# Kernel tuning notes

Measured on AMD Instinct MI355X. Metric: run time of the kernel, lower is better.

## Reference

```python
import jax, jax.numpy as jnp
import numpy as np

B, T_FRAMES, N, D, H, HT = 2, 16, 256, 768, 12, 12
INNER = 2 * D  # ConditionedTransitionBlock expansion_factor=2

def _ln(x, eps=1e-5):
    m = jnp.mean(x, axis=-1, keepdims=True)
    v = jnp.var(x, axis=-1, keepdims=True)
    return (x - m) * jax.lax.rsqrt(v + eps)

def _adaln(a, s, snorm_w, scale_w, scale_b, shift_w):
    an = _ln(a)            # LayerNorm(dim), no affine
    sn = _ln(s) * snorm_w  # LayerNorm(dim_cond), weight only
    return jax.nn.sigmoid(sn @ scale_w + scale_b) * an + sn @ shift_w

def _forward(a, s, bias, timestamps,
             ada_snorm_w, ada_scale_w, ada_scale_b, ada_shift_w,
             pb_q_w, pb_q_b, pb_k_w, pb_v_w, pb_g_w, pb_o_w,
             op_w, op_b,
             tr_snorm_w, tr_scale_w, tr_scale_b, tr_shift_w,
             tr_gate_w, tr_ab_w, tr_ba_w, tr_out_w, tr_out_b,
             tmp_ln_w, tmp_ln_b, tmp_q_w, tmp_q_b, tmp_k_w, tmp_v_w,
             tmp_decay, tmp_o_w,
             mask, multiplicity, T):
    BT, Nn, Dd = a.shape
    Bb = BT // T
    dh = Dd // H
    # --- AdaLN ---
    b = _adaln(a, s, ada_snorm_w, ada_scale_w, ada_scale_b, ada_shift_w)
    # --- pair-bias spatial attention (compute_pair_bias=False: z already (B,N,N,H)) ---
    q = (b @ pb_q_w + pb_q_b).reshape(BT, Nn, H, dh)
    k = (b @ pb_k_w).reshape(BT, Nn, H, dh)
    v = (b @ pb_v_w).reshape(BT, Nn, H, dh)
    z = jnp.transpose(bias, (0, 3, 1, 2))     # (B, H, N, N)
    z = jnp.repeat(z, multiplicity, axis=0)   # expand over T -> (B*T, H, N, N)
    scores = jnp.einsum('bqhd,bkhd->bhqk', q, k) * (dh ** -0.5) + z
    scores = jnp.where(mask[:, None, None, :], scores, -1e6)
    attn = jax.nn.softmax(scores, axis=-1)
    o = jnp.einsum('bhqk,bkhd->bqhd', attn, v).reshape(BT, Nn, Dd)
    g = jax.nn.sigmoid(b @ pb_g_w)
    attn_out = (g * o) @ pb_o_w
    # gated output projection (sigmoid, weights init 0 / bias -2) multiplied into residual
    a = a + jax.nn.sigmoid(s @ op_w + op_b) * attn_out
    # --- temporal attention with decay over T frames ---
    x = a.reshape(Bb, T, Nn, Dd).transpose(0, 2, 1, 3)   # (B, N, T, D)
    h = _ln(x) * tmp_ln_w + tmp_ln_b
    dht = Dd // HT
    qt = (h @ tmp_q_w + tmp_q_b).reshape(Bb, Nn, T, HT, dht)
    kt = (h @ tmp_k_w).reshape(Bb, Nn, T, HT, dht)
    vt = (h @ tmp_v_w).reshape(Bb, Nn, T, HT, dht)
    dt = jnp.abs(timestamps[:, :, None] - timestamps[:, None, :])           # (B, T, T)
    tb = -jax.nn.softplus(tmp_decay)[None, :, None, None] * dt[:, None]     # (B, HT, T, T)
    sct = jnp.einsum('bnqhd,bnkhd->bnhqk', qt, kt) * (dht ** -0.5) + tb[:, None]
    att = jax.nn.softmax(sct, axis=-1)
    ot = jnp.einsum('bnhqk,bnkhd->bnqhd', att, vt).reshape(Bb, Nn, T, Dd) @ tmp_o_w
    x = x + ot  # residual inside temporal attention
    a = x.transpose(0, 2, 1, 3).reshape(BT, Nn, Dd)
    # --- conditioned transition (SwiGLU gated by sigmoid(Linear(s))) ---
    b2 = _adaln(a, s, tr_snorm_w, tr_scale_w, tr_scale_b, tr_shift_w)
    hid = jax.nn.silu(b2 @ tr_gate_w) * (b2 @ tr_ab_w)
    a = a + jax.nn.sigmoid(s @ tr_out_w + tr_out_b) * (hid @ tr_ba_w)
    return a  # post_layer_norm=False -> Identity

def setup_inputs():
    key = jax.random.key(0)
    ks = iter(jax.random.split(key, 48))
    f = lambda shape, sc=1.0: jax.random.normal(next(ks), shape, jnp.float32) * sc
    return {
        'a': f((B * T_FRAMES, N, D)),
        's': f((B * T_FRAMES, N, D)),
        'bias': f((B, N, N, H)),
        'mask': jnp.ones((B * T_FRAMES, N), dtype=bool),
        'timestamps': jnp.sort(jax.random.uniform(next(ks), (B, T_FRAMES)) * 10.0, axis=-1),
        'multiplicity': T_FRAMES,
        'T': T_FRAMES,
        'ada_snorm_w': jnp.ones((D,)), 'ada_scale_w': f((D, D), 0.02),
        'ada_scale_b': jnp.zeros((D,)), 'ada_shift_w': f((D, D), 0.02),
        'pb_q_w': f((D, D), 0.02), 'pb_q_b': jnp.zeros((D,)),
        'pb_k_w': f((D, D), 0.02), 'pb_v_w': f((D, D), 0.02),
        'pb_g_w': f((D, D), 0.02), 'pb_o_w': f((D, D), 0.02),
        'op_w': f((D, D), 0.02), 'op_b': jnp.full((D,), -2.0),
        'tr_snorm_w': jnp.ones((D,)), 'tr_scale_w': f((D, D), 0.02),
        'tr_scale_b': jnp.zeros((D,)), 'tr_shift_w': f((D, D), 0.02),
        'tr_gate_w': f((D, INNER), 0.02), 'tr_ab_w': f((D, INNER), 0.02),
        'tr_ba_w': f((INNER, D), 0.02),
        'tr_out_w': f((D, D), 0.02), 'tr_out_b': jnp.full((D,), -2.0),
        'tmp_ln_w': jnp.ones((D,)), 'tmp_ln_b': jnp.zeros((D,)),
        'tmp_q_w': f((D, D), 0.02), 'tmp_q_b': jnp.zeros((D,)),
        'tmp_k_w': f((D, D), 0.02), 'tmp_v_w': f((D, D), 0.02),
        'tmp_decay': jnp.full((HT,), 0.5), 'tmp_o_w': f((D, D), 0.02),
    }

def reference(a, s, bias, mask, timestamps, multiplicity, T,
              ada_snorm_w, ada_scale_w, ada_scale_b, ada_shift_w,
              pb_q_w, pb_q_b, pb_k_w, pb_v_w, pb_g_w, pb_o_w,
              op_w, op_b,
              tr_snorm_w, tr_scale_w, tr_scale_b, tr_shift_w,
              tr_gate_w, tr_ab_w, tr_ba_w, tr_out_w, tr_out_b,
              tmp_ln_w, tmp_ln_b, tmp_q_w, tmp_q_b, tmp_k_w, tmp_v_w,
              tmp_decay, tmp_o_w):
    return _forward(a, s, bias, timestamps,
                    ada_snorm_w, ada_scale_w, ada_scale_b, ada_shift_w,
                    pb_q_w, pb_q_b, pb_k_w, pb_v_w, pb_g_w, pb_o_w,
                    op_w, op_b,
                    tr_snorm_w, tr_scale_w, tr_scale_b, tr_shift_w,
                    tr_gate_w, tr_ab_w, tr_ba_w, tr_out_w, tr_out_b,
                    tmp_ln_w, tmp_ln_b, tmp_q_w, tmp_q_b, tmp_k_w, tmp_v_w,
                    tmp_decay, tmp_o_w,
                    mask, multiplicity, T)
```

## Files before the change

### kernel.cpp

```cpp
#include <hip/hip_runtime.h>

typedef short s16x8 __attribute__((ext_vector_type(8)));
typedef short s16x4 __attribute__((ext_vector_type(4)));
typedef float f32x4 __attribute__((ext_vector_type(4)));
typedef __bf16 bf16x8 __attribute__((ext_vector_type(8)));

__device__ __forceinline__ float bf2f(short u) {
  union { unsigned int i; float f; } c;
  c.i = ((unsigned int)(unsigned short)u) << 16;
  return c.f;
}
__device__ __forceinline__ short f2bf(float f) {
  union { float f; unsigned int i; } c; c.f = f;
  unsigned int r = c.i + 0x7FFFu + ((c.i >> 16) & 1u);
  return (short)(r >> 16);
}
__device__ __forceinline__ float sigmoidf_(float x) { return 1.f / (1.f + __expf(-x)); }

template <typename T>
__device__ __forceinline__ auto mfma_sel(T a, T b, f32x4 c, int)
    -> decltype(__builtin_amdgcn_mfma_f32_16x16x32_bf16(a, b, c, 0, 0, 0)) {
  return __builtin_amdgcn_mfma_f32_16x16x32_bf16(a, b, c, 0, 0, 0);
}
template <typename T>
__device__ __forceinline__ f32x4 mfma_sel(T a, T b, f32x4 c, long) {
  return __builtin_amdgcn_mfma_f32_16x16x32_bf16(
      __builtin_bit_cast(bf16x8, a), __builtin_bit_cast(bf16x8, b), c, 0, 0, 0);
}
__device__ __forceinline__ f32x4 MFMA16(s16x8 a, s16x8 b, f32x4 c) {
  return mfma_sel(a, b, c, 0);
}

__device__ __forceinline__ void gl2lds16(const void* g, void* l) {
  __builtin_amdgcn_global_load_lds(
      (const __attribute__((address_space(1))) unsigned int*)g,
      (__attribute__((address_space(3))) unsigned int*)l, 16, 0, 0);
}

__device__ __forceinline__ int xcd_swz(int id, int nwg) {
  int q = nwg >> 3, r = nwg & 7;
  int xcd = id & 7, idx = id >> 3;
  return (xcd < r ? xcd * (q + 1) : r * (q + 1) + (xcd - r) * q) + idx;
}

__device__ __forceinline__ void tile_mn(int nid, int gx, int* mt, int* nt) {
  int sb = nid / (gx << 3);
  int rem = nid - sb * (gx << 3);
  *mt = (sb << 3) + (rem & 7);
  *nt = rem >> 3;
}

#define OFF_WADA1    0u
#define OFF_WQKVG    2359296u
#define OFF_WO       7077888u
#define OFF_WGATES   8257536u
#define OFF_WTMPQKV  10616832u
#define OFF_WTMPO    14155776u
#define OFF_WADA2    15335424u
#define OFF_WTRANS   17694720u
#define OFF_WBA      22413312u
#define OFF_BIAS     24772608u
#define OFF_ZT       24812544u
#define OFF_AN1      31104000u
#define OFF_SN1      43686912u
#define OFF_SN2      56269824u
#define OFF_SBF      68852736u
#define OFF_CADA     81435648u
#define OFF_QKVG     106601472u
#define OFF_GATES    156933120u
#define OFF_OGO      182098944u
#define OFF_A1       194681856u

__global__ __launch_bounds__(256) void prep_all(
    const float* p0, const float* p1, const float* p2, const float* p3,
    const float* p4, const float* p5, const float* p6, const float* p7,
    const float* p8, const float* p9, const float* p10, const float* p11,
    const float* p12, const float* p13, const float* p14, const float* p15,
    const float* p16, const float* p17, short* wsb,
    const float* __restrict__ zsrc, const float* __restrict__ ada_scale_b,
    const float* __restrict__ pb_q_b, const float* __restrict__ op_b,
    const float* __restrict__ tr_out_b, const float* __restrict__ tmp_q_b,
    const float* __restrict__ tr_scale_b,
    float* __restrict__ biasbuf, short* __restrict__ zt,
    const float* __restrict__ a_in, const float* __restrict__ s_in,
    const float* __restrict__ lnw1, const float* __restrict__ lnw2,
    short* __restrict__ an1, short* __restrict__ sn1, short* __restrict__ sn2,
    short* __restrict__ sbf) {
  const int z = blockIdx.z;
  const int tid = threadIdx.y * 32 + threadIdx.x;
  if (z < 18) {
    struct E { int K, N, dst; };
    const E tab[18] = {
        {768, 768, 0},        {768, 768, 589824},
        {768, 768, 1179648},  {768, 768, 1769472},
        {768, 768, 2359296},  {768, 768, 2949120},
        {768, 768, 3538944},
        {768, 768, 4128768},  {768, 768, 4718592},
        {768, 768, 7667712},  {768, 768, 8257536},
        {768, 1536, 8847360}, {768, 1536, 10027008},
        {1536, 768, 11206656},
        {768, 768, 5308416},  {768, 768, 5898240}, {768, 768, 6488064},
        {768, 768, 7077888}};
    int K = tab[z].K, N = tab[z].N;
    int n0 = blockIdx.x << 5, k0 = blockIdx.y << 5;
    if (n0 >= N || k0 >= K) return;
    const float* src;
    switch (z) {
      case 0: src = p0; break;  case 1: src = p1; break;
      case 2: src = p2; break;  case 3: src = p3; break;
      case 4: src = p4; break;  case 5: src = p5; break;
      case 6: src = p6; break;  case 7: src = p7; break;
      case 8: src = p8; break;  case 9: src = p9; break;
      case 10: src = p10; break; case 11: src = p11; break;
      case 12: src = p12; break; case 13: src = p13; break;
      case 14: src = p14; break; case 15: src = p15; break;
      case 16: src = p16; break; default: src = p17; break;
    }
    short* dst = wsb + tab[z].dst;
    __shared__ float tile[32][33];
    int tx = threadIdx.x, ty = threadIdx.y;
#pragma unroll
    for (int j = 0; j < 4; j++)
      tile[ty + j * 8][tx] = src[(long)(k0 + ty + j * 8) * N + n0 + tx];
    __syncthreads();
#pragma unroll
    for (int j = 0; j < 4; j++)
      dst[(long)(n0 + ty + j * 8) * K + k0 + tx] = f2bf(tile[tx][ty + j * 8]);
  } else if (z == 18) {
    const int bid = blockIdx.y * 48 + blockIdx.x;
    if (bid < 512) {
      const int b = bid >> 8, qq = bid & 255;
      const float* src = zsrc + (long)bid * 3072 + tid * 12;
      f32x4 v0 = *(const f32x4*)(src);
      f32x4 v1 = *(const f32x4*)(src + 4);
      f32x4 v2 = *(const f32x4*)(src + 8);
      float vals[12] = {v0[0], v0[1], v0[2], v0[3], v1[0], v1[1],
                        v1[2], v1[3], v2[0], v2[1], v2[2], v2[3]};
#pragma unroll
      for (int h = 0; h < 12; h++)
        zt[(((long)(b * 12 + h) * 256 + qq) << 8) + tid] = f2bf(vals[h]);
    } else if (bid < 551) {
      int j = (bid - 512) * 256 + tid;
      if (j < 9984) {
        float v;
        if (j < 1536) v = (j < 768) ? ada_scale_b[j] : 0.f;
        else if (j < 4608) { int jj = j - 1536; v = (jj < 768) ? pb_q_b[jj] : 0.f; }
        else if (j < 6144) { int jj = j - 4608; v = (jj < 768) ? op_b[jj] : tr_out_b[jj - 768]; }
        else if (j < 8448) { int jj = j - 6144; v = (jj < 768) ? tmp_q_b[jj] : 0.f; }
        else { int jj = j - 8448; v = (jj < 768) ? tr_scale_b[jj] : 0.f; }
        biasbuf[j] = v;
      }
    }
  } else {
    const int bid = blockIdx.y * 48 + blockIdx.x;
    if (bid >= 2048) return;
    const int wave = tid >> 6, lane = tid & 63;
    const int row = (bid << 2) + wave;
    const float* ar = a_in + (long)row * 768;
    const float* sr = s_in + (long)row * 768;
    f32x4 av[3], sv[3];
    float s0 = 0, s1 = 0, s2 = 0, s3 = 0;
#pragma unroll
    for (int k = 0; k < 3; k++) {
      int col = (lane << 2) + (k << 8);
      av[k] = *(const f32x4*)(ar + col);
      sv[k] = *(const f32x4*)(sr + col);
#pragma unroll
      for (int e = 0; e < 4; e++) {
        s0 += av[k][e]; s1 += av[k][e] * av[k][e];
        s2 += sv[k][e]; s3 += sv[k][e] * sv[k][e];
      }
    }
#pragma unroll
    for (int o = 32; o; o >>= 1) {
      s0 += __shfl_xor(s0, o, 64); s1 += __shfl_xor(s1, o, 64);
      s2 += __shfl_xor(s2, o, 64); s3 += __shfl_xor(s3, o, 64);
    }
    const float inv768 = 1.f / 768.f;
    float ma = s0 * inv768, va = s1 * inv768 - ma * ma;
    float ia = rsqrtf(va + 1e-5f);
    float ms = s2 * inv768, vs = s3 * inv768 - ms * ms;
    float is_ = rsqrtf(vs + 1e-5f);
#pragma unroll
    for (int k = 0; k < 3; k++) {
      int col = (lane << 2) + (k << 8);
      long o = (long)row * 768 + col;
      s16x4 o1, o2, o3, o4;
#pragma unroll
      for (int e = 0; e < 4; e++) {
        o1[e] = f2bf((av[k][e] - ma) * ia);
        float sn = (sv[k][e] - ms) * is_;
        o2[e] = f2bf(sn * lnw1[col + e]);
        o3[e] = f2bf(sn * lnw2[col + e]);
        o4[e] = f2bf(sv[k][e]);
      }
      *(s16x4*)(an1 + o) = o1;
      *(s16x4*)(sn1 + o) = o2;
      *(s16x4*)(sn2 + o) = o3;
      *(s16x4*)(sbf + o) = o4;
    }
  }
}

__global__ __launch_bounds__(256) void ln_affine(
    const float* __restrict__ in, const float* __restrict__ w,
    const float* __restrict__ b, short* __restrict__ out) {
  const int wave = threadIdx.x >> 6, lane = threadIdx.x & 63;
  const int row = (blockIdx.x << 2) + wave;
  const float* xr = in + (long)row * 768;
  f32x4 xv[3];
  float s0 = 0, s1 = 0;
#pragma unroll
  for (int k = 0; k < 3; k++) {
    int col = (lane << 2) + (k << 8);
    xv[k] = *(const f32x4*)(xr + col);
#pragma unroll
    for (int e = 0; e < 4; e++) { s0 += xv[k][e]; s1 += xv[k][e] * xv[k][e]; }
  }
#pragma unroll
  for (int o = 32; o; o >>= 1) { s0 += __shfl_xor(s0, o, 64); s1 += __shfl_xor(s1, o, 64); }
  const float inv768 = 1.f / 768.f;
  float m = s0 * inv768, v = s1 * inv768 - m * m;
  float inv = rsqrtf(v + 1e-5f);
#pragma unroll
  for (int k = 0; k < 3; k++) {
    int col = (lane << 2) + (k << 8);
    s16x4 p;
#pragma unroll
    for (int e = 0; e < 4; e++) {
      float y = (xv[k][e] - m) * inv;
      if (w) y = y * w[col + e] + b[col + e];
      p[e] = f2bf(y);
    }
    *(s16x4*)(out + (long)row * 768 + col) = p;
  }
}

template <int EP>
__device__ __forceinline__ void dev_gemm_bt(
    short* lds,
    const short* __restrict__ A, const short* __restrict__ W,
    const float* __restrict__ bias, void* __restrict__ Cout,
    const float* __restrict__ res, const short* __restrict__ gate,
    int K, int ldA, int ldC, int gld) {
  const int tid = threadIdx.x;
  const int wave = tid >> 6;
  const int lane = tid & 63;
  const int gx = gridDim.x;
  const int nid = xcd_swz(blockIdx.y * gx + blockIdx.x, gx * gridDim.y);
  int mt_, nt_;
  tile_mn(nid, gx, &mt_, &nt_);
  const int m0 = mt_ << 7;
  const int n0 = nt_ << 7;
  const int wm = (wave & 1) << 6, wn = (wave >> 1) << 6;
  const int q = lane >> 4, r = lane & 15;
  f32x4 acc[4][4];
#pragma unroll
  for (int i = 0; i < 4; i++)
#pragma unroll
    for (int j = 0; j < 4; j++) acc[i][j] = (f32x4){0.f, 0.f, 0.f, 0.f};

  auto stage = [&](short* buf, int kt) {
    short* sA = buf;
    short* sB = buf + 8192;
#pragma unroll
    for (int t = 0; t < 4; t++) {
      int c = (t << 8) + tid;
      int m = c >> 3, kc = (c & 7) ^ (m & 7);
      gl2lds16(A + (long)(m0 + m) * ldA + kt + (kc << 3),
               sA + (((t << 8) + (wave << 6)) << 3));
    }
#pragma unroll
    for (int t = 0; t < 4; t++) {
      int c = (t << 8) + tid;
      int m = c >> 3, kc = (c & 7) ^ (m & 7);
      gl2lds16(W + (long)(n0 + m) * K + kt + (kc << 3),
               sB + (((t << 8) + (wave << 6)) << 3));
    }
  };
  auto compute = [&](const short* buf) {
    const short* sA = buf;
    const short* sB = buf + 8192;
#pragma unroll
    for (int ks = 0; ks < 2; ks++) {
      s16x8 av[4], bv[4];
#pragma unroll
      for (int mt = 0; mt < 4; mt++) {
        int row = wm + (mt << 4) + r;
        int ch = ((ks << 2) + q) ^ (row & 7);
        av[mt] = *(const s16x8*)(sA + ((row << 3) + ch) * 8);
      }
#pragma unroll
      for (int nt = 0; nt < 4; nt++) {
        int row = wn + (nt << 4) + r;
        int ch = ((ks << 2) + q) ^ (row & 7);
        bv[nt] = *(const s16x8*)(sB + ((row << 3) + ch) * 8);
      }
#pragma unroll
      for (int mt = 0; mt < 4; mt++)
#pragma unroll
        for (int nt = 0; nt < 4; nt++)
          acc[mt][nt] = MFMA16(bv[nt], av[mt], acc[mt][nt]);
    }
  };

  short* cb = lds;
  short* nb = lds + 16384;
  stage(cb, 0);
  __syncthreads();
  for (int kt = 64; kt < K; kt += 64) {
    stage(nb, kt);
    compute(cb);
    __syncthreads();
    short* t = cb; cb = nb; nb = t;
  }
  compute(cb);

#pragma unroll
  for (int mt = 0; mt < 4; mt++) {
    const int gm = m0 + wm + (mt << 4) + r;
#pragma unroll
    for (int nt = 0; nt < 4; nt++) {
      const int gnb = n0 + wn + (nt << 4) + (q << 2);
      f32x4 v = acc[mt][nt];
      if (bias) {
        f32x4 b4 = *(const f32x4*)(bias + gnb);
        v += b4;
      }
      long o = (long)gm * ldC + gnb;
      if (EP == 0) {
        s16x4 p;
#pragma unroll
        for (int e = 0; e < 4; e++) p[e] = f2bf(v[e]);
        *(s16x4*)((short*)Cout + o) = p;
      } else if (EP == 1) {
        s16x4 p;
#pragma unroll
        for (int e = 0; e < 4; e++) p[e] = f2bf(sigmoidf_(v[e]));
        *(s16x4*)((short*)Cout + o) = p;
      } else if (EP == 2) {
        f32x4 r4 = *(const f32x4*)(res + o);
        *(f32x4*)((float*)Cout + o) = r4 + v;
      } else {
        f32x4 r4 = *(const f32x4*)(res + o);
        s16x4 g4 = *(const s16x4*)(gate + (long)gm * gld + gnb);
        f32x4 out;
#pragma unroll
        for (int e = 0; e < 4; e++) out[e] = r4[e] + bf2f(g4[e]) * v[e];
        *(f32x4*)((float*)Cout + o) = out;
      }
    }
  }
}

template <int MODE>
__device__ __forceinline__ void dev_gemm_dual(
    short* lds,
    const short* __restrict__ A, const short* __restrict__ W, int woff2,
    const float* __restrict__ bias, const short* __restrict__ an,
    short* __restrict__ out, int ldO) {
  const int tid = threadIdx.x;
  const int wave = tid >> 6, lane = tid & 63;
  const int gx = gridDim.x;
  const int nid = xcd_swz(blockIdx.y * gx + blockIdx.x, gx * gridDim.y);
  int mt_, nt_;
  tile_mn(nid, gx, &mt_, &nt_);
  const int m0 = mt_ << 7;
  const int n0 = nt_ << 6;
  const int wm = (wave & 1) << 6, wn = (wave >> 1) << 5;
  const int q = lane >> 4, r = lane & 15;
  f32x4 acc1[4][2], acc2[4][2];
#pragma unroll
  for (int i = 0; i < 4; i++)
#pragma unroll
    for (int j = 0; j < 2; j++) {
      acc1[i][j] = (f32x4){0.f, 0.f, 0.f, 0.f};
      acc2[i][j] = (f32x4){0.f, 0.f, 0.f, 0.f};
    }

  auto stage = [&](short* buf, int kt) {
    short* sA = buf;
    short* sB1 = buf + 8192;
    short* sB2 = buf + 12288;
#pragma unroll
    for (int t = 0; t < 4; t++) {
      int c = (t << 8) + tid;
      int m = c >> 3, kc = (c & 7) ^ (m & 7);
      gl2lds16(A + (long)(m0 + m) * 768 + kt + (kc << 3),
               sA + (((t << 8) + (wave << 6)) << 3));
    }
#pragma unroll
    for (int t = 0; t < 2; t++) {
      int c = (t << 8) + tid;
      int m = c >> 3, kc = (c & 7) ^ (m & 7);
      gl2lds16(W + (long)(n0 + m) * 768 + kt + (kc << 3),
               sB1 + (((t << 8) + (wave << 6)) << 3));
      gl2lds16(W + (long)(woff2 + n0 + m) * 768 + kt + (kc << 3),
               sB2 + (((t << 8) + (wave << 6)) << 3));
    }
  };
  auto compute = [&](const short* buf) {
    const short* sA = buf;
    const short* sB1 = buf + 8192;
    const short* sB2 = buf + 12288;
#pragma unroll
    for (int ks = 0; ks < 2; ks++) {
      s16x8 av[4], b1[2], b2[2];
#pragma unroll
      for (int mt = 0; mt < 4; mt++) {
        int row = wm + (mt << 4) + r;
        int ch = ((ks << 2) + q) ^ (row & 7);
        av[mt] = *(const s16x8*)(sA + ((row << 3) + ch) * 8);
      }
#pragma unroll
      for (int nt = 0; nt < 2; nt++) {
        int row = wn + (nt << 4) + r;
        int ch = ((ks << 2) + q) ^ (row & 7);
        b1[nt] = *(const s16x8*)(sB1 + ((row << 3) + ch) * 8);
        b2[nt] = *(const s16x8*)(sB2 + ((row << 3) + ch) * 8);
      }
#pragma unroll
      for (int mt = 0; mt < 4; mt++)
#pragma unroll
        for (int nt = 0; nt < 2; nt++) {
          acc1[mt][nt] = MFMA16(b1[nt], av[mt], acc1[mt][nt]);
          acc2[mt][nt] = MFMA16(b2[nt], av[mt], acc2[mt][nt]);
        }
    }
  };

  short* cb = lds;
  short* nb = lds + 16384;
  stage(cb, 0);
  __syncthreads();
  for (int kt = 64; kt < 768; kt += 64) {
    stage(nb, kt);
    compute(cb);
    __syncthreads();
    short* t = cb; cb = nb; nb = t;
  }
  compute(cb);

#pragma unroll
  for (int mt = 0; mt < 4; mt++) {
    const int gm = m0 + wm + (mt << 4) + r;
#pragma unroll
    for (int nt = 0; nt < 2; nt++) {
      const int gnb = n0 + wn + (nt << 4) + (q << 2);
      s16x4 p;
      if (MODE == 0) {
        f32x4 b4 = *(const f32x4*)(bias + gnb);
        s16x4 an4 = *(const s16x4*)(an + (long)gm * 768 + gnb);
#pragma unroll
        for (int e = 0; e < 4; e++)
          p[e] = f2bf(sigmoidf_(acc1[mt][nt][e] + b4[e]) * bf2f(an4[e]) +
                      acc2[mt][nt][e]);
      } else {
#pragma unroll
        for (int e = 0; e < 4; e++) {
          float x = acc1[mt][nt][e];
          p[e] = f2bf(x * sigmoidf_(x) * acc2[mt][nt][e]);
        }
      }
      *(s16x4*)(out + (long)gm * ldO + gnb) = p;
    }
  }
}

template <int EP>
__global__ __launch_bounds__(256) void gemm_bt(
    const short* __restrict__ A, const short* __restrict__ W,
    const float* __restrict__ bias, void* __restrict__ Cout,
    const float* __restrict__ res, const short* __restrict__ gate,
    int K, int ldA, int ldC, int gld) {
  __shared__ short lds[32768];
  dev_gemm_bt<EP>(lds, A, W, bias, Cout, res, gate, K, ldA, ldC, gld);
}

template <int MODE>
__global__ __launch_bounds__(256) void gemm_dual(
    const short* __restrict__ A, const short* __restrict__ W, int woff2,
    const float* __restrict__ bias, const short* __restrict__ an,
    short* __restrict__ out, int ldO) {
  __shared__ short lds[32768];
  dev_gemm_dual<MODE>(lds, A, W, woff2, bias, an, out, ldO);
}

__global__ __launch_bounds__(256) void gemm_pair(
    const short* __restrict__ sbf, const short* __restrict__ wgates,
    const float* __restrict__ bias_g, short* __restrict__ gates,
    const short* __restrict__ sn1, const short* __restrict__ wada1,
    const float* __restrict__ bias_a, const short* __restrict__ an1,
    short* __restrict__ outb) {
  __shared__ short lds[32768];
  if (blockIdx.z == 0)
    dev_gemm_bt<1>(lds, sbf, wgates, bias_g, (void*)gates, nullptr, nullptr,
                   768, 768, 1536, 0);
  else
    dev_gemm_dual<0>(lds, sn1, wada1, 768, bias_a, an1, outb, 768);
}

__global__ __launch_bounds__(256) void attn_spatial(
    const short* __restrict__ qkvg, const short* __restrict__ zt, short* __restrict__ ogo) {
  __shared__ short sKP[256 * 64];
  __shared__ short sVt[64 * 256];
  const int tid = threadIdx.x;
  const int wave = tid >> 6, lane = tid & 63;
  const int qt = blockIdx.x, h = blockIdx.y, bt = blockIdx.z;
  const int b = bt >> 4;
  const int q0 = qt << 6;
  const long rowbase = (long)bt << 8;
  const int hoff = h << 6;

#pragma unroll
  for (int t = 0; t < 8; t++) {
    int c = (t << 8) + tid;
    int tok = c >> 3, kc = (c & 7) ^ (tok & 7);
    *(s16x8*)(sKP + (c << 3)) =
        *(const s16x8*)(qkvg + (rowbase + tok) * 3072 + 768 + hoff + (kc << 3));
  }
#pragma unroll
  for (int t = 0; t < 8; t++) {
    int u = (t << 8) + tid;
    int tok = u >> 3, dc = u & 7;
    s16x8 v8 = *(const s16x8*)(qkvg + (rowbase + tok) * 3072 + 1536 + hoff + (dc << 3));
#pragma unroll
    for (int e = 0; e < 8; e++) {
      int d = (dc << 3) + e;
      int ch = (tok >> 3) ^ (d & 7);
      sVt[((d << 5) + ch) * 8 + (tok & 7)] = v8[e];
    }
  }
  __syncthreads();

  const int q = lane >> 4, cc = lane & 15;
  f32x4 acc[16];
#pragma unroll
  for (int i = 0; i < 16; i++) acc[i] = (f32x4){0.f, 0.f, 0.f, 0.f};
  {
    const int arow = (wave << 4) + cc;
    const short* qrow = qkvg + (rowbase + q0 + arow) * 3072 + hoff;
#pragma unroll
    for (int ks = 0; ks < 2; ks++) {
      s16x8 av = *(const s16x8*)(qrow + (ks << 5) + (q << 3));
#pragma unroll
      for (int nt = 0; nt < 16; nt++) {
        int tok = (nt << 4) + cc;
        int chb = ((ks << 2) + q) ^ (tok & 7);
        s16x8 bv = *(const s16x8*)(sKP + ((tok << 3) + chb) * 8);
        acc[nt] = MFMA16(av, bv, acc[nt]);
      }
    }
  }
  const short* ztb = zt + (((long)(b * 12 + h) * 256 + q0 + (wave << 4)) << 8);
#pragma unroll
  for (int reg = 0; reg < 4; reg++) {
    int lr = (q << 2) + reg;
    float mx = -3.0e38f;
#pragma unroll
    for (int nt = 0; nt < 16; nt++) {
      float v = acc[nt][reg] * 0.125f + bf2f(ztb[lr * 256 + (nt << 4) + cc]);
      acc[nt][reg] = v;
      mx = fmaxf(mx, v);
    }
    mx = fmaxf(mx, __shfl_xor(mx, 1, 16));
    mx = fmaxf(mx, __shfl_xor(mx, 2, 16));
    mx = fmaxf(mx, __shfl_xor(mx, 4, 16));
    mx = fmaxf(mx, __shfl_xor(mx, 8, 16));
    float sum = 0.f;
#pragma unroll
    for (int nt = 0; nt < 16; nt++) {
      float e = __expf(acc[nt][reg] - mx);
      acc[nt][reg] = e; sum += e;
    }
    sum += __shfl_xor(sum, 1, 16);
    sum += __shfl_xor(sum, 2, 16);
    sum += __shfl_xor(sum, 4, 16);
    sum += __shfl_xor(sum, 8, 16);
    float inv = 1.f / sum;
#pragma unroll
    for (int nt = 0; nt < 16; nt++) acc[nt][reg] *= inv;
  }
  __syncthreads();
#pragma unroll
  for (int nt = 0; nt < 16; nt++) {
#pragma unroll
    for (int reg = 0; reg < 4; reg++) {
      int rP = (wave << 4) + (q << 2) + reg;
      int col = (nt << 4) + cc;
      int ch = (col >> 3) ^ (rP & 7);
      sKP[((rP << 5) + ch) * 8 + (col & 7)] = f2bf(acc[nt][reg]);
    }
  }
  __syncthreads();
  f32x4 oacc[4];
#pragma unroll
  for (int i = 0; i < 4; i++) oacc[i] = (f32x4){0.f, 0.f, 0.f, 0.f};
  const int prow = (wave << 4) + cc;
#pragma unroll
  for (int ksi = 0; ksi < 8; ksi++) {
    int cha = ((ksi << 2) + q) ^ (prow & 7);
    s16x8 pa = *(const s16x8*)(sKP + ((prow << 5) + cha) * 8);
#pragma unroll
    for (int dt = 0; dt < 4; dt++) {
      int d = (dt << 4) + cc;
      int chv = ((ksi << 2) + q) ^ (d & 7);
      s16x8 bv = *(const s16x8*)(sVt + ((d << 5) + chv) * 8);
      oacc[dt] = MFMA16(pa, bv, oacc[dt]);
    }
  }
#pragma unroll
  for (int dt = 0; dt < 4; dt++) {
#pragma unroll
    for (int reg = 0; reg < 4; reg++) {
      int rowt = q0 + (wave << 4) + (q << 2) + reg;
      int dcol = (dt << 4) + cc;
      long grow = rowbase + rowt;
      float gl = bf2f(qkvg[grow * 3072 + 2304 + hoff + dcol]);
      ogo[grow * 768 + hoff + dcol] = f2bf(oacc[dt][reg] * sigmoidf_(gl));
    }
  }
}

__global__ __launch_bounds__(256) void attn_temporal(
    const short* __restrict__ qkvt, const float* __restrict__ ts,
    const float* __restrict__ decay_raw, short* __restrict__ out) {
  __shared__ short sKV[16 * 1544];
  const int bn = blockIdx.x;
  const int b = bn >> 8, n = bn & 255;
  const int tid = threadIdx.x;
#pragma unroll
  for (int t = 0; t < 12; t++) {
    int u = t * 256 + tid;
    int row = u / 192, cc = u % 192;
    *(s16x8*)(sKV + row * 1544 + cc * 8) =
        *(const s16x8*)(qkvt + ((long)(b * 16 + row) * 256 + n) * 2304 + 768 + cc * 8);
  }
  __syncthreads();
  const int h = tid >> 4, tq = tid & 15;
  if (h < 12) {
    const int hoff = h << 6;
    float dec = log1pf(__expf(decay_raw[h]));
    float tsq = ts[b * 16 + tq];
    s16x8 qv[8];
    const short* qrow = qkvt + ((long)(b * 16 + tq) * 256 + n) * 2304 + hoff;
#pragma unroll
    for (int dc = 0; dc < 8; dc++) qv[dc] = *(const s16x8*)(qrow + dc * 8);
    float sc[16];
#pragma unroll
    for (int tk = 0; tk < 16; tk++) {
      float dot = 0.f;
#pragma unroll
      for (int dc = 0; dc < 8; dc++) {
        s16x8 kv = *(const s16x8*)(sKV + tk * 1544 + hoff + dc * 8);
#pragma unroll
        for (int e = 0; e < 8; e++) dot += bf2f(qv[dc][e]) * bf2f(kv[e]);
      }
      sc[tk] = dot * 0.125f - dec * fabsf(tsq - ts[b * 16 + tk]);
    }
    float mx = sc[0];
#pragma unroll
    for (int tk = 1; tk < 16; tk++) mx = fmaxf(mx, sc[tk]);
    float sum = 0.f;
#pragma unroll
    for (int tk = 0; tk < 16; tk++) { sc[tk] = __expf(sc[tk] - mx); sum += sc[tk]; }
    float inv = 1.f / sum;
    float oa[64];
#pragma unroll
    for (int d = 0; d < 64; d++) oa[d] = 0.f;
#pragma unroll
    for (int tk = 0; tk < 16; tk++) {
      float wgt = sc[tk] * inv;
#pragma unroll
      for (int dc = 0; dc < 8; dc++) {
        s16x8 vv = *(const s16x8*)(sKV + tk * 1544 + 768 + hoff + dc * 8);
#pragma unroll
        for (int e = 0; e < 8; e++) oa[dc * 8 + e] += wgt * bf2f(vv[e]);
      }
    }
    long orow = (long)(b * 16 + tq) * 256 + n;
#pragma unroll
    for (int dc = 0; dc < 8; dc++) {
      s16x8 o8;
#pragma unroll
      for (int e = 0; e < 8; e++) o8[e] = f2bf(oa[dc * 8 + e]);
      *(s16x8*)(out + orow * 768 + hoff + dc * 8) = o8;
    }
  }
}

extern "C" void kernel_launch(void* const* d_in, const int* in_sizes, int n_in,
                              void* d_out, int out_size, void* d_ws, size_t ws_size,
                              hipStream_t stream) {
  (void)in_sizes; (void)n_in; (void)out_size; (void)ws_size;
  const float* a_in      = (const float*)d_in[0];
  const float* s_in      = (const float*)d_in[1];
  const float* bias_in   = (const float*)d_in[2];
  const float* ts        = (const float*)d_in[4];
  const float* ada_snorm = (const float*)d_in[7];
  const float* ada_scale_w = (const float*)d_in[8];
  const float* ada_scale_b = (const float*)d_in[9];
  const float* ada_shift_w = (const float*)d_in[10];
  const float* pb_q_w = (const float*)d_in[11];
  const float* pb_q_b = (const float*)d_in[12];
  const float* pb_k_w = (const float*)d_in[13];
  const float* pb_v_w = (const float*)d_in[14];
  const float* pb_g_w = (const float*)d_in[15];
  const float* pb_o_w = (const float*)d_in[16];
  const float* op_w = (const float*)d_in[17];
  const float* op_b = (const float*)d_in[18];
  const float* tr_snorm = (const float*)d_in[19];
  const float* tr_scale_w = (const float*)d_in[20];
  const float* tr_scale_b = (const float*)d_in[21];
  const float* tr_shift_w = (const float*)d_in[22];
  const float* tr_gate_w = (const float*)d_in[23];
  const float* tr_ab_w = (const float*)d_in[24];
  const float* tr_ba_w = (const float*)d_in[25];
  const float* tr_out_w = (const float*)d_in[26];
  const float* tr_out_b = (const float*)d_in[27];
  const float* tmp_ln_w = (const float*)d_in[28];
  const float* tmp_ln_b = (const float*)d_in[29];
  const float* tmp_q_w = (const float*)d_in[30];
  const float* tmp_q_b = (const float*)d_in[31];
  const float* tmp_k_w = (const float*)d_in[32];
  const float* tmp_v_w = (const float*)d_in[33];
  const float* tmp_decay = (const float*)d_in[34];
  const float* tmp_o_w = (const float*)d_in[35];

  char* ws = (char*)d_ws;
  short* W16 = (short*)ws;
  short* WADA1 = (short*)(ws + OFF_WADA1);
  short* WQKVG = (short*)(ws + OFF_WQKVG);
  short* WO = (short*)(ws + OFF_WO);
  short* WGATES = (short*)(ws + OFF_WGATES);
  short* WTMPQKV = (short*)(ws + OFF_WTMPQKV);
  short* WTMPO = (short*)(ws + OFF_WTMPO);
  short* WADA2 = (short*)(ws + OFF_WADA2);
  short* WTRANS = (short*)(ws + OFF_WTRANS);
  short* WBA = (short*)(ws + OFF_WBA);
  float* BIASB = (float*)(ws + OFF_BIAS);
  short* ZT = (short*)(ws + OFF_ZT);
  short* AN1 = (short*)(ws + OFF_AN1);
  short* SN1 = (short*)(ws + OFF_SN1);
  short* SN2 = (short*)(ws + OFF_SN2);
  short* SBF = (short*)(ws + OFF_SBF);
  short* CADA = (short*)(ws + OFF_CADA);
  short* QKVG = (short*)(ws + OFF_QKVG);
  short* GATES = (short*)(ws + OFF_GATES);
  short* OGO = (short*)(ws + OFF_OGO);
  float* A1F = (float*)(ws + OFF_A1);
  float* OUTF = (float*)d_out;

  prep_all<<<dim3(48, 48, 20), dim3(32, 8, 1), 0, stream>>>(
      ada_scale_w, ada_shift_w, pb_q_w, pb_k_w, pb_v_w, pb_g_w, pb_o_w,
      op_w, tr_out_w, tr_scale_w, tr_shift_w, tr_gate_w, tr_ab_w, tr_ba_w,
      tmp_q_w, tmp_k_w, tmp_v_w, tmp_o_w, W16,
      bias_in, ada_scale_b, pb_q_b, op_b, tr_out_b, tmp_q_b, tr_scale_b,
      BIASB, ZT,
      a_in, s_in, ada_snorm, tr_snorm, AN1, SN1, SN2, SBF);
  gemm_pair<<<dim3(12, 64, 2), 256, 0, stream>>>(
      SBF, WGATES, BIASB + 4608, GATES, SN1, WADA1, BIASB + 0, AN1, SBF);
  gemm_bt<0><<<dim3(24, 64), 256, 0, stream>>>(SBF, WQKVG, BIASB + 1536, QKVG,
                                               nullptr, nullptr, 768, 768, 3072, 0);
  attn_spatial<<<dim3(4, 12, 32), 256, 0, stream>>>(QKVG, ZT, OGO);
  gemm_bt<3><<<dim3(6, 64), 256, 0, stream>>>(OGO, WO, nullptr, A1F, a_in, GATES,
                                              768, 768, 768, 1536);
  ln_affine<<<2048, 256, 0, stream>>>(A1F, tmp_ln_w, tmp_ln_b, AN1);
  gemm_bt<0><<<dim3(18, 64), 256, 0, stream>>>(AN1, WTMPQKV, BIASB + 6144, QKVG,
                                               nullptr, nullptr, 768, 768, 2304, 0);
  attn_temporal<<<512, 256, 0, stream>>>(QKVG, ts, tmp_decay, OGO);
  gemm_bt<2><<<dim3(6, 64), 256, 0, stream>>>(OGO, WTMPO, nullptr, A1F, A1F, nullptr,
                                              768, 768, 768, 0);
  ln_affine<<<2048, 256, 0, stream>>>(A1F, nullptr, nullptr, SN1);
  gemm_dual<0><<<dim3(12, 64), 256, 0, stream>>>(SN2, WADA2, 768, BIASB + 8448, SN1,
                                                 SBF, 768);
  gemm_dual<1><<<dim3(24, 64), 256, 0, stream>>>(SBF, WTRANS, 1536, nullptr, nullptr,
                                                 CADA, 1536);
  gemm_bt<3><<<dim3(6, 64), 256, 0, stream>>>(CADA, WBA, nullptr, OUTF, A1F,
                                              GATES + 768, 1536, 1536, 768, 1536);
}
```

Measured before the change: 614.8 us.

## Restructure GEMM kernels to 8 waves with interleaved load/MFMA pipeline

The bt and dual GEMM kernels move from 256 to 512 threads per block, so each wave owns a smaller N slice, and the main loop is rebuilt. Global-to-LDS loads for the next tile are split into A and B units and issued between MFMA phases. Explicit vmcnt waits and raw barriers replace __syncthreads, and s_setprio raises wave priority around the MFMA bursts. The aim is better overlap of memory and matrix work and more waves to hide latency, at the cost of more LDS read traffic per MFMA and tighter register limits from launch_bounds(512,4).

Result: no change. 613.4 us (-0.2%).

```diff
diff --git a/kernel.cpp b/kernel.cpp
--- a/kernel.cpp
+++ b/kernel.cpp
@@ -36,6 +36,12 @@
       (const __attribute__((address_space(1))) unsigned int*)g,
       (__attribute__((address_space(3))) unsigned int*)l, 16, 0, 0);
 }
+
+#define WAIT_VM2()  asm volatile("s_waitcnt vmcnt(2)" ::: "memory")
+#define WAIT_VM0()  asm volatile("s_waitcnt vmcnt(0)" ::: "memory")
+#define BAR()       __builtin_amdgcn_s_barrier()
+#define PRIO1()     __builtin_amdgcn_s_setprio(1)
+#define PRIO0()     __builtin_amdgcn_s_setprio(0)
 
 __device__ __forceinline__ int xcd_swz(int id, int nwg) {
   int q = nwg >> 3, r = nwg & 7;
@@ -252,75 +258,105 @@
   tile_mn(nid, gx, &mt_, &nt_);
   const int m0 = mt_ << 7;
   const int n0 = nt_ << 7;
-  const int wm = (wave & 1) << 6, wn = (wave >> 1) << 6;
+  const int wm = (wave & 1) << 6;
+  const int wn = (wave >> 1) << 5;
   const int q = lane >> 4, r = lane & 15;
-  f32x4 acc[4][4];
+  f32x4 acc[4][2];
 #pragma unroll
   for (int i = 0; i < 4; i++)
 #pragma unroll
-    for (int j = 0; j < 4; j++) acc[i][j] = (f32x4){0.f, 0.f, 0.f, 0.f};
-
-  auto stage = [&](short* buf, int kt) {
-    short* sA = buf;
-    short* sB = buf + 8192;
-#pragma unroll
-    for (int t = 0; t < 4; t++) {
-      int c = (t << 8) + tid;
-      int m = c >> 3, kc = (c & 7) ^ (m & 7);
-      gl2lds16(A + (long)(m0 + m) * ldA + kt + (kc << 3),
-               sA + (((t << 8) + (wave << 6)) << 3));
-    }
-#pragma unroll
-    for (int t = 0; t < 4; t++) {
-      int c = (t << 8) + tid;
-      int m = c >> 3, kc = (c & 7) ^ (m & 7);
-      gl2lds16(W + (long)(n0 + m) * K + kt + (kc << 3),
-               sB + (((t << 8) + (wave << 6)) << 3));
-    }
-  };
-  auto compute = [&](const short* buf) {
-    const short* sA = buf;
-    const short* sB = buf + 8192;
+    for (int j = 0; j < 2; j++) acc[i][j] = (f32x4){0.f, 0.f, 0.f, 0.f};
+
+  const short* pA[2];
+  const short* pB[2];
+#pragma unroll
+  for (int j = 0; j < 2; j++) {
+    int c = (j << 9) + tid;
+    int m = c >> 3, kc = (c & 7) ^ (m & 7);
+    pA[j] = A + (long)(m0 + m) * ldA + (kc << 3);
+    pB[j] = W + (long)(n0 + m) * K + (kc << 3);
+  }
+  const int lA0 = (wave << 9);
+  const int lA1 = (1 << 12) + (wave << 9);
+  const int lB0 = 8192 + (wave << 9);
+  const int lB1 = 8192 + (1 << 12) + (wave << 9);
+
+  int offA[4][2], offB[2][2];
+#pragma unroll
+  for (int p = 0; p < 4; p++)
 #pragma unroll
     for (int ks = 0; ks < 2; ks++) {
-      s16x8 av[4], bv[4];
-#pragma unroll
-      for (int mt = 0; mt < 4; mt++) {
-        int row = wm + (mt << 4) + r;
-        int ch = ((ks << 2) + q) ^ (row & 7);
-        av[mt] = *(const s16x8*)(sA + ((row << 3) + ch) * 8);
-      }
-#pragma unroll
-      for (int nt = 0; nt < 4; nt++) {
-        int row = wn + (nt << 4) + r;
-        int ch = ((ks << 2) + q) ^ (row & 7);
-        bv[nt] = *(const s16x8*)(sB + ((row << 3) + ch) * 8);
-      }
-#pragma unroll
-      for (int mt = 0; mt < 4; mt++)
-#pragma unroll
-        for (int nt = 0; nt < 4; nt++)
-          acc[mt][nt] = MFMA16(bv[nt], av[mt], acc[mt][nt]);
-    }
-  };
-
-  short* cb = lds;
-  short* nb = lds + 16384;
-  stage(cb, 0);
-  __syncthreads();
-  for (int kt = 64; kt < K; kt += 64) {
-    stage(nb, kt);
-    compute(cb);
-    __syncthreads();
-    short* t = cb; cb = nb; nb = t;
-  }
-  compute(cb);
+      int row = wm + (p << 4) + r;
+      offA[p][ks] = ((row << 3) + (((ks << 2) + q) ^ (row & 7))) << 3;
+    }
+#pragma unroll
+  for (int ks = 0; ks < 2; ks++)
+#pragma unroll
+    for (int nt = 0; nt < 2; nt++) {
+      int row = wn + (nt << 4) + r;
+      offB[ks][nt] = 8192 + (((row << 3) + (((ks << 2) + q) ^ (row & 7))) << 3);
+    }
+
+  auto unitA = [&](short* buf, int ko) {
+    gl2lds16(pA[0] + ko, buf + lA0);
+    gl2lds16(pA[1] + ko, buf + lA1);
+  };
+  auto unitB = [&](short* buf, int ko) {
+    gl2lds16(pB[0] + ko, buf + lB0);
+    gl2lds16(pB[1] + ko, buf + lB1);
+  };
+
+  s16x8 bv[2][2];
+  auto loadbv = [&](const short* buf) {
+#pragma unroll
+    for (int ks = 0; ks < 2; ks++)
+#pragma unroll
+      for (int nt = 0; nt < 2; nt++)
+        bv[ks][nt] = *(const s16x8*)(buf + offB[ks][nt]);
+  };
+  auto phase = [&](const short* buf, int p) {
+    s16x8 a0 = *(const s16x8*)(buf + offA[p][0]);
+    s16x8 a1 = *(const s16x8*)(buf + offA[p][1]);
+    PRIO1();
+#pragma unroll
+    for (int nt = 0; nt < 2; nt++) {
+      acc[p][nt] = MFMA16(bv[0][nt], a0, acc[p][nt]);
+      acc[p][nt] = MFMA16(bv[1][nt], a1, acc[p][nt]);
+    }
+    PRIO0();
+  };
+
+  auto TILE = [&](const short* cur, short* nxt, int ko) {
+    unitA(nxt, ko);
+    WAIT_VM2(); BAR();
+    loadbv(cur);
+    phase(cur, 0);
+    unitB(nxt, ko);
+    phase(cur, 1);
+    phase(cur, 2);
+    phase(cur, 3);
+    BAR();
+  };
+
+  short* b0 = lds;
+  short* b1 = lds + 16384;
+  const int NT = K >> 6;
+  unitA(b0, 0); unitB(b0, 0);
+  int t = 0;
+  for (; t + 2 < NT; t += 2) {
+    TILE(b0, b1, (t + 1) << 6);
+    TILE(b1, b0, (t + 2) << 6);
+  }
+  TILE(b0, b1, (t + 1) << 6);
+  WAIT_VM0(); BAR();
+  loadbv(b1);
+  phase(b1, 0); phase(b1, 1); phase(b1, 2); phase(b1, 3);
 
 #pragma unroll
   for (int mt = 0; mt < 4; mt++) {
     const int gm = m0 + wm + (mt << 4) + r;
 #pragma unroll
-    for (int nt = 0; nt < 4; nt++) {
+    for (int nt = 0; nt < 2; nt++) {
       const int gnb = n0 + wn + (nt << 4) + (q << 2);
       f32x4 v = acc[mt][nt];
       if (bias) {
@@ -367,108 +403,127 @@
   tile_mn(nid, gx, &mt_, &nt_);
   const int m0 = mt_ << 7;
   const int n0 = nt_ << 6;
-  const int wm = (wave & 1) << 6, wn = (wave >> 1) << 5;
+  const int wm = (wave & 1) << 6;
+  const int wn = (wave >> 1) << 4;
   const int q = lane >> 4, r = lane & 15;
-  f32x4 acc1[4][2], acc2[4][2];
-#pragma unroll
-  for (int i = 0; i < 4; i++)
-#pragma unroll
-    for (int j = 0; j < 2; j++) {
-      acc1[i][j] = (f32x4){0.f, 0.f, 0.f, 0.f};
-      acc2[i][j] = (f32x4){0.f, 0.f, 0.f, 0.f};
-    }
-
-  auto stage = [&](short* buf, int kt) {
-    short* sA = buf;
-    short* sB1 = buf + 8192;
-    short* sB2 = buf + 12288;
-#pragma unroll
-    for (int t = 0; t < 4; t++) {
-      int c = (t << 8) + tid;
-      int m = c >> 3, kc = (c & 7) ^ (m & 7);
-      gl2lds16(A + (long)(m0 + m) * 768 + kt + (kc << 3),
-               sA + (((t << 8) + (wave << 6)) << 3));
-    }
-#pragma unroll
-    for (int t = 0; t < 2; t++) {
-      int c = (t << 8) + tid;
-      int m = c >> 3, kc = (c & 7) ^ (m & 7);
-      gl2lds16(W + (long)(n0 + m) * 768 + kt + (kc << 3),
-               sB1 + (((t << 8) + (wave << 6)) << 3));
-      gl2lds16(W + (long)(woff2 + n0 + m) * 768 + kt + (kc << 3),
-               sB2 + (((t << 8) + (wave << 6)) << 3));
-    }
-  };
-  auto compute = [&](const short* buf) {
-    const short* sA = buf;
-    const short* sB1 = buf + 8192;
-    const short* sB2 = buf + 12288;
+  f32x4 acc1[4], acc2[4];
+#pragma unroll
+  for (int i = 0; i < 4; i++) {
+    acc1[i] = (f32x4){0.f, 0.f, 0.f, 0.f};
+    acc2[i] = (f32x4){0.f, 0.f, 0.f, 0.f};
+  }
+
+  const short* pA[2];
+  const short* pB1;
+  const short* pB2;
+#pragma unroll
+  for (int j = 0; j < 2; j++) {
+    int c = (j << 9) + tid;
+    int m = c >> 3, kc = (c & 7) ^ (m & 7);
+    pA[j] = A + (long)(m0 + m) * 768 + (kc << 3);
+  }
+  {
+    int m = tid >> 3, kc = (tid & 7) ^ (m & 7);
+    pB1 = W + (long)(n0 + m) * 768 + (kc << 3);
+    pB2 = W + (long)(woff2 + n0 + m) * 768 + (kc << 3);
+  }
+  const int lA0 = (wave << 9);
+  const int lA1 = (1 << 12) + (wave << 9);
+  const int lB1o = 8192 + (wave << 9);
+  const int lB2o = 12288 + (wave << 9);
+
+  int offA[4][2], offB[2];
+#pragma unroll
+  for (int p = 0; p < 4; p++)
 #pragma unroll
     for (int ks = 0; ks < 2; ks++) {
-      s16x8 av[4], b1[2], b2[2];
-#pragma unroll
-      for (int mt = 0; mt < 4; mt++) {
-        int row = wm + (mt << 4) + r;
-        int ch = ((ks << 2) + q) ^ (row & 7);
-        av[mt] = *(const s16x8*)(sA + ((row << 3) + ch) * 8);
-      }
-#pragma unroll
-      for (int nt = 0; nt < 2; nt++) {
-        int row = wn + (nt << 4) + r;
-        int ch = ((ks << 2) + q) ^ (row & 7);
-        b1[nt] = *(const s16x8*)(sB1 + ((row << 3) + ch) * 8);
-        b2[nt] = *(const s16x8*)(sB2 + ((row << 3) + ch) * 8);
-      }
-#pragma unroll
-      for (int mt = 0; mt < 4; mt++)
-#pragma unroll
-        for (int nt = 0; nt < 2; nt++) {
-          acc1[mt][nt] = MFMA16(b1[nt], av[mt], acc1[mt][nt]);
-          acc2[mt][nt] = MFMA16(b2[nt], av[mt], acc2[mt][nt]);
-        }
-    }
-  };
-
-  short* cb = lds;
-  short* nb = lds + 16384;
-  stage(cb, 0);
-  __syncthreads();
-  for (int kt = 64; kt < 768; kt += 64) {
-    stage(nb, kt);
-    compute(cb);
-    __syncthreads();
-    short* t = cb; cb = nb; nb = t;
-  }
-  compute(cb);
+      int row = wm + (p << 4) + r;
+      offA[p][ks] = ((row << 3) + (((ks << 2) + q) ^ (row & 7))) << 3;
+    }
+#pragma unroll
+  for (int ks = 0; ks < 2; ks++) {
+    int row = wn + r;
+    offB[ks] = ((row << 3) + (((ks << 2) + q) ^ (row & 7))) << 3;
+  }
+
+  auto unitA = [&](short* buf, int ko) {
+    gl2lds16(pA[0] + ko, buf + lA0);
+    gl2lds16(pA[1] + ko, buf + lA1);
+  };
+  auto unitB = [&](short* buf, int ko) {
+    gl2lds16(pB1 + ko, buf + lB1o);
+    gl2lds16(pB2 + ko, buf + lB2o);
+  };
+
+  s16x8 b1v[2], b2v[2];
+  auto loadbv = [&](const short* buf) {
+#pragma unroll
+    for (int ks = 0; ks < 2; ks++) {
+      b1v[ks] = *(const s16x8*)(buf + 8192 + offB[ks]);
+      b2v[ks] = *(const s16x8*)(buf + 12288 + offB[ks]);
+    }
+  };
+  auto phase = [&](const short* buf, int p) {
+    s16x8 a0 = *(const s16x8*)(buf + offA[p][0]);
+    s16x8 a1 = *(const s16x8*)(buf + offA[p][1]);
+    PRIO1();
+    acc1[p] = MFMA16(b1v[0], a0, acc1[p]);
+    acc1[p] = MFMA16(b1v[1], a1, acc1[p]);
+    acc2[p] = MFMA16(b2v[0], a0, acc2[p]);
+    acc2[p] = MFMA16(b2v[1], a1, acc2[p]);
+    PRIO0();
+  };
+  auto TILE = [&](const short* cur, short* nxt, int ko) {
+    unitA(nxt, ko);
+    WAIT_VM2(); BAR();
+    loadbv(cur);
+    phase(cur, 0);
+    unitB(nxt, ko);
+    phase(cur, 1);
+    phase(cur, 2);
+    phase(cur, 3);
+    BAR();
+  };
+
+  short* bb0 = lds;
+  short* bb1 = lds + 16384;
+  const int NT = 12;
+  unitA(bb0, 0); unitB(bb0, 0);
+  int t = 0;
+  for (; t + 2 < NT; t += 2) {
+    TILE(bb0, bb1, (t + 1) << 6);
+    TILE(bb1, bb0, (t + 2) << 6);
+  }
+  TILE(bb0, bb1, (t + 1) << 6);
+  WAIT_VM0(); BAR();
+  loadbv(bb1);
+  phase(bb1, 0); phase(bb1, 1); phase(bb1, 2); phase(bb1, 3);
 
 #pragma unroll
   for (int mt = 0; mt < 4; mt++) {
     const int gm = m0 + wm + (mt << 4) + r;
-#pragma unroll
-    for (int nt = 0; nt < 2; nt++) {
-      const int gnb = n0 + wn + (nt << 4) + (q << 2);
-      s16x4 p;
-      if (MODE == 0) {
-        f32x4 b4 = *(const f32x4*)(bias + gnb);
-        s16x4 an4 = *(const s16x4*)(an + (long)gm * 768 + gnb);
-#pragma unroll
-        for (int e = 0; e < 4; e++)
-          p[e] = f2bf(sigmoidf_(acc1[mt][nt][e] + b4[e]) * bf2f(an4[e]) +
-                      acc2[mt][nt][e]);
-      } else {
-#pragma unroll
-        for (int e = 0; e < 4; e++) {
-          float x = acc1[mt][nt][e];
-          p[e] = f2bf(x * sigmoidf_(x) * acc2[mt][nt][e]);
-        }
+    const int gnb = n0 + wn + (q << 2);
+    s16x4 p;
+    if (MODE == 0) {
+      f32x4 b4 = *(const f32x4*)(bias + gnb);
+      s16x4 an4 = *(const s16x4*)(an + (long)gm * 768 + gnb);
+#pragma unroll
+      for (int e = 0; e < 4; e++)
+        p[e] = f2bf(sigmoidf_(acc1[mt][e] + b4[e]) * bf2f(an4[e]) +
+                    acc2[mt][e]);
+    } else {
+#pragma unroll
+      for (int e = 0; e < 4; e++) {
+        float x = acc1[mt][e];
+        p[e] = f2bf(x * sigmoidf_(x) * acc2[mt][e]);
       }
-      *(s16x4*)(out + (long)gm * ldO + gnb) = p;
-    }
+    }
+    *(s16x4*)(out + (long)gm * ldO + gnb) = p;
   }
 }
 
 template <int EP>
-__global__ __launch_bounds__(256) void gemm_bt(
+__global__ __launch_bounds__(512, 4) void gemm_bt(
     const short* __restrict__ A, const short* __restrict__ W,
     const float* __restrict__ bias, void* __restrict__ Cout,
     const float* __restrict__ res, const short* __restrict__ gate,
@@ -478,7 +533,7 @@
 }
 
 template <int MODE>
-__global__ __launch_bounds__(256) void gemm_dual(
+__global__ __launch_bounds__(512, 4) void gemm_dual(
     const short* __restrict__ A, const short* __restrict__ W, int woff2,
     const float* __restrict__ bias, const short* __restrict__ an,
     short* __restrict__ out, int ldO) {
@@ -486,7 +541,7 @@
   dev_gemm_dual<MODE>(lds, A, W, woff2, bias, an, out, ldO);
 }
 
-__global__ __launch_bounds__(256) void gemm_pair(
+__global__ __launch_bounds__(512, 4) void gemm_pair(
     const short* __restrict__ sbf, const short* __restrict__ wgates,
     const float* __restrict__ bias_g, short* __restrict__ gates,
     const short* __restrict__ sn1, const short* __restrict__ wada1,
@@ -758,24 +813,24 @@
       bias_in, ada_scale_b, pb_q_b, op_b, tr_out_b, tmp_q_b, tr_scale_b,
       BIASB, ZT,
       a_in, s_in, ada_snorm, tr_snorm, AN1, SN1, SN2, SBF);
-  gemm_pair<<<dim3(12, 64, 2), 256, 0, stream>>>(
+  gemm_pair<<<dim3(12, 64, 2), 512, 0, stream>>>(
       SBF, WGATES, BIASB + 4608, GATES, SN1, WADA1, BIASB + 0, AN1, SBF);
-  gemm_bt<0><<<dim3(24, 64), 256, 0, stream>>>(SBF, WQKVG, BIASB + 1536, QKVG,
+  gemm_bt<0><<<dim3(24, 64), 512, 0, stream>>>(SBF, WQKVG, BIASB + 1536, QKVG,
                                                nullptr, nullptr, 768, 768, 3072, 0);
   attn_spatial<<<dim3(4, 12, 32), 256, 0, stream>>>(QKVG, ZT, OGO);
-  gemm_bt<3><<<dim3(6, 64), 256, 0, stream>>>(OGO, WO, nullptr, A1F, a_in, GATES,
+  gemm_bt<3><<<dim3(6, 64), 512, 0, stream>>>(OGO, WO, nullptr, A1F, a_in, GATES,
                                               768, 768, 768, 1536);
   ln_affine<<<2048, 256, 0, stream>>>(A1F, tmp_ln_w, tmp_ln_b, AN1);
-  gemm_bt<0><<<dim3(18, 64), 256, 0, stream>>>(AN1, WTMPQKV, BIASB + 6144, QKVG,
+  gemm_bt<0><<<dim3(18, 64), 512, 0, stream>>>(AN1, WTMPQKV, BIASB + 6144, QKVG,
                                                nullptr, nullptr, 768, 768, 2304, 0);
   attn_temporal<<<512, 256, 0, stream>>>(QKVG, ts, tmp_decay, OGO);
-  gemm_bt<2><<<dim3(6, 64), 256, 0, stream>>>(OGO, WTMPO, nullptr, A1F, A1F, nullptr,
+  gemm_bt<2><<<dim3(6, 64), 512, 0, stream>>>(OGO, WTMPO, nullptr, A1F, A1F, nullptr,
                                               768, 768, 768, 0);
   ln_affine<<<2048, 256, 0, stream>>>(A1F, nullptr, nullptr, SN1);
-  gemm_dual<0><<<dim3(12, 64), 256, 0, stream>>>(SN2, WADA2, 768, BIASB + 8448, SN1,
+  gemm_dual<0><<<dim3(12, 64), 512, 0, stream>>>(SN2, WADA2, 768, BIASB + 8448, SN1,
                                                  SBF, 768);
-  gemm_dual<1><<<dim3(24, 64), 256, 0, stream>>>(SBF, WTRANS, 1536, nullptr, nullptr,
+  gemm_dual<1><<<dim3(24, 64), 512, 0, stream>>>(SBF, WTRANS, 1536, nullptr, nullptr,
                                                  CADA, 1536);
-  gemm_bt<3><<<dim3(6, 64), 256, 0, stream>>>(CADA, WBA, nullptr, OUTF, A1F,
+  gemm_bt<3><<<dim3(6, 64), 512, 0, stream>>>(CADA, WBA, nullptr, OUTF, A1F,
                                               GATES + 768, 1536, 1536, 768, 1536);
 }
```
